# Performance work log

Hardware: AMD Instinct MI355X
Metric: run time of the kernel (lower is better)

## Reference

```python
import jax, jax.numpy as jnp
import numpy as np


def setup_inputs() -> dict:
    key = jax.random.key(0)
    k1, k2 = jax.random.split(key)
    embedding = jax.random.normal(k1, (8192, 256), dtype=jnp.float32)
    label = jax.random.randint(k2, (8192,), 0, 1000, dtype=jnp.int64 if jax.config.jax_enable_x64 else jnp.int32)
    return {"embedding": embedding, "label": label}


def reference(embedding, label):
    # embedding: [B, W]; label is unused by the original module's math.
    B, W = embedding.shape
    miu = embedding.mean(axis=0)                      # [W]
    ec = embedding - miu                              # [B, W] centered
    # mean over batch of outer products ec[b] ec[b]^T == (ec^T @ ec) / B
    cov = jnp.einsum('bi,bj->ij', ec, ec) / B         # [W, W]
    diff = cov - jnp.eye(W, dtype=embedding.dtype)
    loss = jnp.sqrt(jnp.sum(diff * diff))             # Frobenius norm
    return loss
```

## Files before the change

kernel.cpp:

```cpp
#include <hip/hip_runtime.h>
#include <math.h>

typedef unsigned int uint32;
typedef unsigned short ushort16;
typedef __bf16 bf16x8 __attribute__((ext_vector_type(8)));
typedef float f32x16 __attribute__((ext_vector_type(16)));

#define BROWS 8192
#define WDIM 256
#define NT 3
#define CHUNKS 64
#define CHUNK_K 128
#define TILE_ELEMS 16384
#define FIN_BLOCKS 192

#define WS_LOSS 8192
#define WS_DONE 8193
#define WS_PART 8448
#define WS_ET   3154176

__device__ __forceinline__ uint32 pack2bf(float lo, float hi) {
    uint32 a = __float_as_uint(lo), b = __float_as_uint(hi);
    a = (a + 0x7FFFu + ((a >> 16) & 1u)) >> 16;
    b = (b + 0x7FFFu + ((b >> 16) & 1u)) >> 16;
    return a | (b << 16);
}

__global__ __launch_bounds__(256)
void cast_t_kernel(const float* __restrict__ E, float* __restrict__ ws) {
    const int cg = blockIdx.x;
    const int rg = blockIdx.y;
    const int tid = threadIdx.x;
    __shared__ uint32 U[64 * 129];
    __shared__ float Cs[16 * 64];

    if (cg == 0 && rg == 0 && tid < 2) ws[WS_LOSS + tid] = 0.0f;

    const int c4 = tid & 15;
    const int rp = tid >> 4;
    const float* Eb = E + (size_t)(rg * 256) * WDIM + cg * 64;

    float4 cs = make_float4(0.f, 0.f, 0.f, 0.f);
    #pragma unroll
    for (int p = 0; p < 8; ++p) {
        const int rpi = rp + 16 * p;
        const int r0 = 2 * rpi;
        const float4 fa = *(const float4*)(Eb + (size_t)r0 * WDIM + c4 * 4);
        const float4 fb = *(const float4*)(Eb + (size_t)(r0 + 1) * WDIM + c4 * 4);
        cs.x += fa.x + fb.x; cs.y += fa.y + fb.y;
        cs.z += fa.z + fb.z; cs.w += fa.w + fb.w;
        U[(c4 * 4 + 0) * 129 + rpi] = pack2bf(fa.x, fb.x);
        U[(c4 * 4 + 1) * 129 + rpi] = pack2bf(fa.y, fb.y);
        U[(c4 * 4 + 2) * 129 + rpi] = pack2bf(fa.z, fb.z);
        U[(c4 * 4 + 3) * 129 + rpi] = pack2bf(fa.w, fb.w);
    }
    *(float4*)&Cs[rp * 64 + c4 * 4] = cs;
    __syncthreads();

    if (tid < 64) {
        float s = 0.f;
        #pragma unroll
        for (int r = 0; r < 16; ++r) s += Cs[r * 64 + tid];
        ws[rg * WDIM + cg * 64 + tid] = s;
    }

    uint32* Et = (uint32*)(ws + WS_ET);
    const int col = tid >> 2, sub = tid & 3;
    uint32* dstc = Et + (size_t)(cg * 64 + col) * 4096 + rg * 128 + sub * 32;
    const uint32* Uc = U + col * 129 + sub * 32;
    #pragma unroll
    for (int j = 0; j < 8; ++j) {
        uint4 v;
        v.x = Uc[4 * j + 0]; v.y = Uc[4 * j + 1];
        v.z = Uc[4 * j + 2]; v.w = Uc[4 * j + 3];
        *(uint4*)(dstc + 4 * j) = v;
    }
}

__global__ __launch_bounds__(256)
void gram_kernel(float* __restrict__ ws) {
    const ushort16* Et = (const ushort16*)(ws + WS_ET);
    float* partials = ws + WS_PART;
    const int t = blockIdx.x, c = blockIdx.y;
    const int ti = (t == 2) ? 1 : 0;
    const int tj = (t == 0) ? 0 : 1;
    const int tid = threadIdx.x, w = tid >> 6, l = tid & 63;
    const int lm = l & 31;
    const int lk = (l >> 5) * 8;
    const size_t CS = 8192;

    const ushort16* ap = Et + (size_t)(ti * 128 + w * 32 + lm) * CS + (size_t)c * CHUNK_K + lk;
    const ushort16* bp = Et + (size_t)(tj * 128 + lm) * CS + (size_t)c * CHUNK_K + lk;

    f32x16 acc[4];
    #pragma unroll
    for (int n = 0; n < 4; ++n)
        #pragma unroll
        for (int r = 0; r < 16; ++r) acc[n][r] = 0.f;

    #pragma unroll
    for (int s = 0; s < 8; ++s) {
        const int o = s * 16;
        const bf16x8 a  = *(const bf16x8*)(ap + o);
        const bf16x8 b0 = *(const bf16x8*)(bp + o);
        const bf16x8 b1 = *(const bf16x8*)(bp + 32 * CS + o);
        const bf16x8 b2 = *(const bf16x8*)(bp + 64 * CS + o);
        const bf16x8 b3 = *(const bf16x8*)(bp + 96 * CS + o);
        acc[0] = __builtin_amdgcn_mfma_f32_32x32x16_bf16(a, b0, acc[0], 0, 0, 0);
        acc[1] = __builtin_amdgcn_mfma_f32_32x32x16_bf16(a, b1, acc[1], 0, 0, 0);
        acc[2] = __builtin_amdgcn_mfma_f32_32x32x16_bf16(a, b2, acc[2], 0, 0, 0);
        acc[3] = __builtin_amdgcn_mfma_f32_32x32x16_bf16(a, b3, acc[3], 0, 0, 0);
    }

    float* dst = partials + ((size_t)c * NT + t) * TILE_ELEMS;
    const int rbase = 32 * w + 4 * (l >> 5);
    #pragma unroll
    for (int n = 0; n < 4; ++n)
        #pragma unroll
        for (int r = 0; r < 16; ++r) {
            const int row = rbase + (r & 3) + 8 * (r >> 2);
            dst[row * 128 + n * 32 + lm] = acc[n][r];
        }
}

__global__ __launch_bounds__(256)
void finalize_kernel(float* __restrict__ ws, float* __restrict__ out) {
    __shared__ float mu[WDIM];
    __shared__ float red[4];
    const float* partials = ws + WS_PART;
    float* lossacc = ws + WS_LOSS;
    unsigned* done = (unsigned*)(ws + WS_DONE);
    const int tid = threadIdx.x;

    {
        float s = 0.f;
        #pragma unroll 8
        for (int rg = 0; rg < 32; ++rg) s += ws[rg * WDIM + tid];
        mu[tid] = s * (1.0f / (float)BROWS);
    }
    __syncthreads();

    const int e = blockIdx.x * 256 + tid;
    const int t = e >> 14, local = e & 16383;
    const int ti = (t == 2) ? 1 : 0;
    const int tj = (t == 0) ? 0 : 1;
    const int i = ti * 128 + (local >> 7);
    const int j = tj * 128 + (local & 127);

    float g = 0.f;
    #pragma unroll 8
    for (int c = 0; c < CHUNKS; ++c)
        g += partials[((size_t)c * NT + t) * TILE_ELEMS + local];

    const float diff = g * (1.0f / (float)BROWS) - mu[i] * mu[j] - ((i == j) ? 1.0f : 0.0f);
    float v = ((t == 1) ? 2.0f : 1.0f) * diff * diff;

    #pragma unroll
    for (int o = 32; o > 0; o >>= 1) v += __shfl_down(v, o, 64);
    if ((tid & 63) == 0) red[tid >> 6] = v;
    __syncthreads();
    if (tid == 0) {
        atomicAdd(lossacc, red[0] + red[1] + red[2] + red[3]);
        __threadfence();
        const unsigned old = atomicAdd(done, 1u);
        if (old == FIN_BLOCKS - 1) {
            __threadfence();
            out[0] = sqrtf(atomicAdd(lossacc, 0.0f));
        }
    }
}

extern "C" void kernel_launch(void* const* d_in, const int* in_sizes, int n_in,
                              void* d_out, int out_size, void* d_ws, size_t ws_size,
                              hipStream_t stream) {
    const float* E = (const float*)d_in[0];
    float* out = (float*)d_out;
    float* ws = (float*)d_ws;

    cast_t_kernel<<<dim3(4, 32), 256, 0, stream>>>(E, ws);
    gram_kernel<<<dim3(NT, CHUNKS), 256, 0, stream>>>(ws);
    finalize_kernel<<<FIN_BLOCKS, 256, 0, stream>>>(ws, out);
}
```

Before: 83.43 us.

## Fuse bf16 cast into gram kernel via swizzled LDS and store bf16 partials

Removes the separate cast/transpose kernel: each gram block loads its fp32 row chunk, packs it to bf16 into a XOR-swizzled shared buffer, computes column sums from it, and runs MFMA directly from LDS. Partial Gram tiles are written as bf16 instead of fp32, halving partial-buffer traffic for the finalize pass. This removes a launch and a global round trip of the transposed copy, at the cost of re-reading input per tile and reduced precision in partials and means.

```diff
diff --git a/kernel.cpp b/kernel.cpp
--- a/kernel.cpp
+++ b/kernel.cpp
@@ -2,7 +2,7 @@
 #include <math.h>
 
 typedef unsigned int uint32;
-typedef unsigned short ushort16;
+typedef unsigned short u16;
 typedef __bf16 bf16x8 __attribute__((ext_vector_type(8)));
 typedef float f32x16 __attribute__((ext_vector_type(16)));
 
@@ -10,87 +10,79 @@
 #define WDIM 256
 #define NT 3
 #define CHUNKS 64
-#define CHUNK_K 128
 #define TILE_ELEMS 16384
 #define FIN_BLOCKS 192
 
-#define WS_LOSS 8192
-#define WS_DONE 8193
-#define WS_PART 8448
-#define WS_ET   3154176
+#define WS_LOSS 16384
+#define WS_DONE 16385
+#define WS_PART 16640
 
 __device__ __forceinline__ uint32 pack2bf(float lo, float hi) {
     uint32 a = __float_as_uint(lo), b = __float_as_uint(hi);
     a = (a + 0x7FFFu + ((a >> 16) & 1u)) >> 16;
     b = (b + 0x7FFFu + ((b >> 16) & 1u)) >> 16;
-    return a | (b << 16);
+    return (a & 0xFFFFu) | (b << 16);
+}
+__device__ __forceinline__ u16 f2bf(float x) {
+    uint32 a = __float_as_uint(x);
+    return (u16)((a + 0x7FFFu + ((a >> 16) & 1u)) >> 16);
+}
+__device__ __forceinline__ float bflo(uint32 v) { return __uint_as_float(v << 16); }
+__device__ __forceinline__ float bfhi(uint32 v) { return __uint_as_float(v & 0xFFFF0000u); }
+
+__device__ __forceinline__ int uswz(int col, int krp) {
+    return col * 64 + ((((krp >> 2) ^ (col & 15)) << 2) | (krp & 3));
 }
 
 __global__ __launch_bounds__(256)
-void cast_t_kernel(const float* __restrict__ E, float* __restrict__ ws) {
-    const int cg = blockIdx.x;
-    const int rg = blockIdx.y;
+void gram_fused(const float* __restrict__ E, float* __restrict__ ws) {
+    __shared__ uint32 U[WDIM * 64];
+    const int t = blockIdx.x, c = blockIdx.y;
     const int tid = threadIdx.x;
-    __shared__ uint32 U[64 * 129];
-    __shared__ float Cs[16 * 64];
+    const int ncg = (t == 1) ? 4 : 2;
+    const int gcol0 = (t == 2) ? 128 : 0;
+    const int row0 = c * 128;
+    const int c4 = tid & 15, rp = tid >> 4;
 
-    if (cg == 0 && rg == 0 && tid < 2) ws[WS_LOSS + tid] = 0.0f;
+    if (t == 0 && c == 0 && tid < 2) ws[WS_LOSS + tid] = 0.0f;
 
-    const int c4 = tid & 15;
-    const int rp = tid >> 4;
-    const float* Eb = E + (size_t)(rg * 256) * WDIM + cg * 64;
-
-    float4 cs = make_float4(0.f, 0.f, 0.f, 0.f);
-    #pragma unroll
-    for (int p = 0; p < 8; ++p) {
-        const int rpi = rp + 16 * p;
-        const int r0 = 2 * rpi;
-        const float4 fa = *(const float4*)(Eb + (size_t)r0 * WDIM + c4 * 4);
-        const float4 fb = *(const float4*)(Eb + (size_t)(r0 + 1) * WDIM + c4 * 4);
-        cs.x += fa.x + fb.x; cs.y += fa.y + fb.y;
-        cs.z += fa.z + fb.z; cs.w += fa.w + fb.w;
-        U[(c4 * 4 + 0) * 129 + rpi] = pack2bf(fa.x, fb.x);
-        U[(c4 * 4 + 1) * 129 + rpi] = pack2bf(fa.y, fb.y);
-        U[(c4 * 4 + 2) * 129 + rpi] = pack2bf(fa.z, fb.z);
-        U[(c4 * 4 + 3) * 129 + rpi] = pack2bf(fa.w, fb.w);
+    for (int cg = 0; cg < ncg; ++cg) {
+        const float* Eb = E + (size_t)row0 * WDIM + gcol0 + cg * 64;
+        float4 fa[4], fb[4];
+        #pragma unroll
+        for (int p = 0; p < 4; ++p) {
+            const int r0 = 2 * (rp + 16 * p);
+            fa[p] = *(const float4*)(Eb + (size_t)r0 * WDIM + c4 * 4);
+            fb[p] = *(const float4*)(Eb + (size_t)(r0 + 1) * WDIM + c4 * 4);
+        }
+        #pragma unroll
+        for (int p = 0; p < 4; ++p) {
+            const int krp = rp + 16 * p;
+            const int colb = cg * 64 + c4 * 4;
+            const float av[4] = {fa[p].x, fa[p].y, fa[p].z, fa[p].w};
+            const float bv[4] = {fb[p].x, fb[p].y, fb[p].z, fb[p].w};
+            #pragma unroll
+            for (int i = 0; i < 4; ++i)
+                U[uswz(colb + i, krp)] = pack2bf(av[i], bv[i]);
+        }
     }
-    *(float4*)&Cs[rp * 64 + c4 * 4] = cs;
     __syncthreads();
 
-    if (tid < 64) {
+    if (t == 1) {
+        const int col = tid;
         float s = 0.f;
         #pragma unroll
-        for (int r = 0; r < 16; ++r) s += Cs[r * 64 + tid];
-        ws[rg * WDIM + cg * 64 + tid] = s;
+        for (int g = 0; g < 16; ++g) {
+            const uint4 v = *(const uint4*)&U[col * 64 + ((g ^ (col & 15)) << 2)];
+            s += bflo(v.x) + bfhi(v.x) + bflo(v.y) + bfhi(v.y)
+               + bflo(v.z) + bfhi(v.z) + bflo(v.w) + bfhi(v.w);
+        }
+        ws[c * WDIM + col] = s;
     }
 
-    uint32* Et = (uint32*)(ws + WS_ET);
-    const int col = tid >> 2, sub = tid & 3;
-    uint32* dstc = Et + (size_t)(cg * 64 + col) * 4096 + rg * 128 + sub * 32;
-    const uint32* Uc = U + col * 129 + sub * 32;
-    #pragma unroll
-    for (int j = 0; j < 8; ++j) {
-        uint4 v;
-        v.x = Uc[4 * j + 0]; v.y = Uc[4 * j + 1];
-        v.z = Uc[4 * j + 2]; v.w = Uc[4 * j + 3];
-        *(uint4*)(dstc + 4 * j) = v;
-    }
-}
-
-__global__ __launch_bounds__(256)
-void gram_kernel(float* __restrict__ ws) {
-    const ushort16* Et = (const ushort16*)(ws + WS_ET);
-    float* partials = ws + WS_PART;
-    const int t = blockIdx.x, c = blockIdx.y;
-    const int ti = (t == 2) ? 1 : 0;
-    const int tj = (t == 0) ? 0 : 1;
-    const int tid = threadIdx.x, w = tid >> 6, l = tid & 63;
-    const int lm = l & 31;
-    const int lk = (l >> 5) * 8;
-    const size_t CS = 8192;
-
-    const ushort16* ap = Et + (size_t)(ti * 128 + w * 32 + lm) * CS + (size_t)c * CHUNK_K + lk;
-    const ushort16* bp = Et + (size_t)(tj * 128 + lm) * CS + (size_t)c * CHUNK_K + lk;
+    const int w = tid >> 6, l = tid & 63, lm = l & 31;
+    const int bBase = (t == 1) ? 128 : 0;
+    const int colA = w * 32 + lm;
 
     f32x16 acc[4];
     #pragma unroll
@@ -99,27 +91,26 @@
         for (int r = 0; r < 16; ++r) acc[n][r] = 0.f;
 
     #pragma unroll
-    for (int s = 0; s < 8; ++s) {
-        const int o = s * 16;
-        const bf16x8 a  = *(const bf16x8*)(ap + o);
-        const bf16x8 b0 = *(const bf16x8*)(bp + o);
-        const bf16x8 b1 = *(const bf16x8*)(bp + 32 * CS + o);
-        const bf16x8 b2 = *(const bf16x8*)(bp + 64 * CS + o);
-        const bf16x8 b3 = *(const bf16x8*)(bp + 96 * CS + o);
-        acc[0] = __builtin_amdgcn_mfma_f32_32x32x16_bf16(a, b0, acc[0], 0, 0, 0);
-        acc[1] = __builtin_amdgcn_mfma_f32_32x32x16_bf16(a, b1, acc[1], 0, 0, 0);
-        acc[2] = __builtin_amdgcn_mfma_f32_32x32x16_bf16(a, b2, acc[2], 0, 0, 0);
-        acc[3] = __builtin_amdgcn_mfma_f32_32x32x16_bf16(a, b3, acc[3], 0, 0, 0);
+    for (int s8 = 0; s8 < 8; ++s8) {
+        const int grp = 2 * s8 + (l >> 5);
+        const bf16x8 a = *(const bf16x8*)&U[colA * 64 + ((grp ^ (colA & 15)) << 2)];
+        #pragma unroll
+        for (int n = 0; n < 4; ++n) {
+            const int colB = bBase + n * 32 + lm;
+            const bf16x8 b = *(const bf16x8*)&U[colB * 64 + ((grp ^ (colB & 15)) << 2)];
+            acc[n] = __builtin_amdgcn_mfma_f32_32x32x16_bf16(a, b, acc[n], 0, 0, 0);
+        }
     }
 
-    float* dst = partials + ((size_t)c * NT + t) * TILE_ELEMS;
+    u16* part = (u16*)(ws + WS_PART);
+    u16* dst = part + ((size_t)c * NT + t) * TILE_ELEMS;
     const int rbase = 32 * w + 4 * (l >> 5);
     #pragma unroll
     for (int n = 0; n < 4; ++n)
         #pragma unroll
         for (int r = 0; r < 16; ++r) {
             const int row = rbase + (r & 3) + 8 * (r >> 2);
-            dst[row * 128 + n * 32 + lm] = acc[n][r];
+            dst[row * 128 + n * 32 + lm] = f2bf(acc[n][r]);
         }
 }
 
@@ -127,7 +118,7 @@
 void finalize_kernel(float* __restrict__ ws, float* __restrict__ out) {
     __shared__ float mu[WDIM];
     __shared__ float red[4];
-    const float* partials = ws + WS_PART;
+    const u16* part = (const u16*)(ws + WS_PART);
     float* lossacc = ws + WS_LOSS;
     unsigned* done = (unsigned*)(ws + WS_DONE);
     const int tid = threadIdx.x;
@@ -135,7 +126,7 @@
     {
         float s = 0.f;
         #pragma unroll 8
-        for (int rg = 0; rg < 32; ++rg) s += ws[rg * WDIM + tid];
+        for (int c = 0; c < CHUNKS; ++c) s += ws[c * WDIM + tid];
         mu[tid] = s * (1.0f / (float)BROWS);
     }
     __syncthreads();
@@ -150,7 +141,7 @@
     float g = 0.f;
     #pragma unroll 8
     for (int c = 0; c < CHUNKS; ++c)
-        g += partials[((size_t)c * NT + t) * TILE_ELEMS + local];
+        g += bflo((uint32)part[((size_t)c * NT + t) * TILE_ELEMS + local]);
 
     const float diff = g * (1.0f / (float)BROWS) - mu[i] * mu[j] - ((i == j) ? 1.0f : 0.0f);
     float v = ((t == 1) ? 2.0f : 1.0f) * diff * diff;
@@ -177,7 +168,6 @@
     float* out = (float*)d_out;
     float* ws = (float*)d_ws;
 
-    cast_t_kernel<<<dim3(4, 32), 256, 0, stream>>>(E, ws);
-    gram_kernel<<<dim3(NT, CHUNKS), 256, 0, stream>>>(ws);
+    gram_fused<<<dim3(NT, CHUNKS), 256, 0, stream>>>(E, ws);
     finalize_kernel<<<FIN_BLOCKS, 256, 0, stream>>>(ws, out);
 }
```

Measured after the change: 76.03 us. 8.9% less time.
